# Performance work log

Measured on AMD Instinct MI355X. Metric: run time of the kernel, lower is better.

The kernel has to match this reference:

```python
import jax, jax.numpy as jnp
import numpy as np

N, C, S = 2, 512, 256
SCALE = 2.0

def setup_inputs() -> dict:
    key = jax.random.key(0)
    kq, kk, kv = jax.random.split(key, 3)
    q = jax.random.normal(kq, (N, C, S), dtype=jnp.float32)
    k = jax.random.normal(kk, (N, C, S), dtype=jnp.float32)
    v = jax.random.normal(kv, (N, C, S), dtype=jnp.float32)
    return {"q": q, "k": k, "v": v}

def reference(q, k, v):
    # q: (N,C,S) -> (N,C,1,S); k: (N,C,S) -> (N,1,C,S)
    # weights[n,c,d] = -sum_s |k[n,d,s] - q[n,c,s]| / scale
    diff = jnp.abs(k[:, None, :, :] - q[:, :, None, :])  # (N,C,C,S)
    weights = -(diff / SCALE).sum(axis=-1)               # (N,C,C)
    weights = jax.nn.softmax(weights, axis=-1)
    rep = jnp.einsum('ncd,nds->ncs', weights, v)         # (N,C,S)
    return rep
```

## Files before the change

kernel.cpp:

```cpp
#include <hip/hip_runtime.h>
#include <hip/hip_bf16.h>


constexpr int N_ = 2;
constexpr int C_ = 512;
constexpr int S_ = 256;
constexpr int TC = 4;
constexpr int NW = 4;

template <int CTRL, int ROW_MASK>
__device__ __forceinline__ float dpp_add(float x) {
    int yi = __builtin_amdgcn_update_dpp(0, __float_as_int(x), CTRL, ROW_MASK, 0xf, true);
    return x + __int_as_float(yi);
}
template <int CTRL, int ROW_MASK>
__device__ __forceinline__ float dpp_max(float x) {
    int yi = __builtin_amdgcn_update_dpp(__float_as_int(x), __float_as_int(x), CTRL, ROW_MASK, 0xf, false);
    return fmaxf(x, __int_as_float(yi));
}
__device__ __forceinline__ float dpp_reduce_halves(float x) {
    x = dpp_add<0x111, 0xf>(x);
    x = dpp_add<0x112, 0xf>(x);
    x = dpp_add<0x114, 0xf>(x);
    x = dpp_add<0x118, 0xf>(x);
    x = dpp_add<0x142, 0xa>(x);
    return x;
}
__device__ __forceinline__ float wave_sum_bcast(float x) {
    x = dpp_reduce_halves(x);
    x = dpp_add<0x143, 0xc>(x);
    return __int_as_float(__builtin_amdgcn_readlane(__float_as_int(x), 63));
}
__device__ __forceinline__ float wave_max_bcast(float x) {
    x = dpp_max<0x111, 0xf>(x);
    x = dpp_max<0x112, 0xf>(x);
    x = dpp_max<0x114, 0xf>(x);
    x = dpp_max<0x118, 0xf>(x);
    x = dpp_max<0x142, 0xa>(x);
    x = dpp_max<0x143, 0xc>(x);
    return __int_as_float(__builtin_amdgcn_readlane(__float_as_int(x), 63));
}

template <int DSPLIT>
__global__ __launch_bounds__(256, 4)
void laplace_attn_main(const float* __restrict__ q,
                       const float* __restrict__ k,
                       const float* __restrict__ v,
                       float* __restrict__ ws) {
    constexpr int DH  = C_ / DSPLIT;
    constexpr int DPW = DH / NW;
    constexpr int E   = DH / 64;
    constexpr size_t PO_SZ = (size_t)N_ * C_ * DSPLIT * S_;
    constexpr size_t ST_SZ = (size_t)N_ * C_ * DSPLIT;

    const int b      = blockIdx.x;
    constexpr int per_n = (C_ / TC) * DSPLIT;
    const int n    = b / per_n;
    const int r    = b - n * per_n;
    const int half = r % DSPLIT;
    const int c0   = (r / DSPLIT) * TC;
    const int tid  = threadIdx.x;
    const int w    = tid >> 6;
    const int lane = tid & 63;

    const float* kbase = k + (size_t)n * C_ * S_;
    const float* vbase = v + (size_t)n * C_ * S_;

    float* po = ws;
    float* pm = ws + PO_SZ;
    float* pl = pm + ST_SZ;

    __shared__ float4 wt[DH];
    __shared__ float4 accs[NW][TC][64];

    const int h = lane >> 5;
    const int j = lane & 31;
    float4 qa[TC], qb[TC];
    #pragma unroll
    for (int c = 0; c < TC; ++c) {
        const float4* qr = (const float4*)(q + ((size_t)n * C_ + c0 + c) * S_);
        qa[c] = qr[2 * j];
        qb[c] = qr[2 * j + 1];
    }

    const int dw0 = half * DH + w * DPW;
    const float* kw = kbase + (size_t)dw0 * S_;

    #pragma unroll 2
    for (int g2 = 0; g2 < DPW; g2 += 2) {
        const float4* rp = (const float4*)(kw + (size_t)(g2 + h) * S_ + j * 8);
        const float4 ka = rp[0];
        const float4 kb = rp[1];
        float s0[TC], s1[TC];
        #pragma unroll
        for (int c = 0; c < TC; ++c) {
            float p = fabsf(ka.x - qa[c].x) + fabsf(ka.y - qa[c].y)
                    + fabsf(ka.z - qa[c].z) + fabsf(ka.w - qa[c].w)
                    + fabsf(kb.x - qb[c].x) + fabsf(kb.y - qb[c].y)
                    + fabsf(kb.z - qb[c].z) + fabsf(kb.w - qb[c].w);
            p = dpp_reduce_halves(p);
            s0[c] = __int_as_float(__builtin_amdgcn_readlane(__float_as_int(p), 31));
            s1[c] = __int_as_float(__builtin_amdgcn_readlane(__float_as_int(p), 63));
        }
        if (lane == 0) {
            wt[w * DPW + g2]     = make_float4(-0.5f * s0[0], -0.5f * s0[1],
                                               -0.5f * s0[2], -0.5f * s0[3]);
            wt[w * DPW + g2 + 1] = make_float4(-0.5f * s1[0], -0.5f * s1[1],
                                               -0.5f * s1[2], -0.5f * s1[3]);
        }
    }
    __syncthreads();

    {
        const float* wtf = (const float*)wt;
        float x[E];
        #pragma unroll
        for (int e = 0; e < E; ++e) x[e] = wtf[(lane + 64 * e) * 4 + w];
        float m = x[0];
        #pragma unroll
        for (int e = 1; e < E; ++e) m = fmaxf(m, x[e]);
        m = wave_max_bcast(m);
        float es[E], l = 0.f;
        #pragma unroll
        for (int e = 0; e < E; ++e) { es[e] = __expf(x[e] - m); l += es[e]; }
        l = wave_sum_bcast(l);
        float* wtm = (float*)wt;
        #pragma unroll
        for (int e = 0; e < E; ++e) wtm[(lane + 64 * e) * 4 + w] = es[e];
        if (lane == 0) {
            const size_t sidx = ((size_t)n * C_ + c0 + w) * DSPLIT + half;
            pm[sidx] = m;
            pl[sidx] = l;
        }
    }
    __syncthreads();

    float4 acc[TC];
    #pragma unroll
    for (int c = 0; c < TC; ++c) acc[c] = make_float4(0.f, 0.f, 0.f, 0.f);

    const float4* v4 = (const float4*)(vbase + (size_t)dw0 * S_);
    #pragma unroll 4
    for (int dd = 0; dd < DPW; ++dd) {
        const float4 vv = v4[dd * 64 + lane];
        const float4 ww = wt[w * DPW + dd];
        acc[0].x += ww.x * vv.x; acc[0].y += ww.x * vv.y;
        acc[0].z += ww.x * vv.z; acc[0].w += ww.x * vv.w;
        acc[1].x += ww.y * vv.x; acc[1].y += ww.y * vv.y;
        acc[1].z += ww.y * vv.z; acc[1].w += ww.y * vv.w;
        acc[2].x += ww.z * vv.x; acc[2].y += ww.z * vv.y;
        acc[2].z += ww.z * vv.z; acc[2].w += ww.z * vv.w;
        acc[3].x += ww.w * vv.x; acc[3].y += ww.w * vv.y;
        acc[3].z += ww.w * vv.z; acc[3].w += ww.w * vv.w;
    }
    #pragma unroll
    for (int c = 0; c < TC; ++c) accs[w][c][lane] = acc[c];
    __syncthreads();

    {
        const int c = w;
        float4 a  = accs[0][c][lane];
        float4 bq = accs[1][c][lane];
        float4 cc = accs[2][c][lane];
        float4 dq = accs[3][c][lane];
        float4 o;
        o.x = (a.x + bq.x) + (cc.x + dq.x);
        o.y = (a.y + bq.y) + (cc.y + dq.y);
        o.z = (a.z + bq.z) + (cc.z + dq.z);
        o.w = (a.w + bq.w) + (cc.w + dq.w);
        const size_t oidx = (((size_t)n * C_ + c0 + c) * DSPLIT + half) * S_;
        ((float4*)(po + oidx))[lane] = o;
    }
}

template <int DSPLIT>
__global__ __launch_bounds__(64)
void laplace_attn_combine(const float* __restrict__ ws,
                          float* __restrict__ out) {
    constexpr size_t PO_SZ = (size_t)N_ * C_ * DSPLIT * S_;
    constexpr size_t ST_SZ = (size_t)N_ * C_ * DSPLIT;
    const int b    = blockIdx.x;
    const int lane = threadIdx.x;

    const float* po = ws;
    const float* pm = ws + PO_SZ;
    const float* pl = pm + ST_SZ;

    float m[DSPLIT], l[DSPLIT];
    #pragma unroll
    for (int hh = 0; hh < DSPLIT; ++hh) {
        m[hh] = pm[(size_t)b * DSPLIT + hh];
        l[hh] = pl[(size_t)b * DSPLIT + hh];
    }
    float M = m[0];
    #pragma unroll
    for (int hh = 1; hh < DSPLIT; ++hh) M = fmaxf(M, m[hh]);
    float den = 0.f, a[DSPLIT];
    #pragma unroll
    for (int hh = 0; hh < DSPLIT; ++hh) { a[hh] = __expf(m[hh] - M); den += a[hh] * l[hh]; }
    const float inv = 1.f / den;

    float4 rsum = make_float4(0.f, 0.f, 0.f, 0.f);
    #pragma unroll
    for (int hh = 0; hh < DSPLIT; ++hh) {
        const float4 o = ((const float4*)(po + ((size_t)b * DSPLIT + hh) * S_))[lane];
        rsum.x += a[hh] * o.x;
        rsum.y += a[hh] * o.y;
        rsum.z += a[hh] * o.z;
        rsum.w += a[hh] * o.w;
    }
    float4 rr;
    rr.x = rsum.x * inv; rr.y = rsum.y * inv;
    rr.z = rsum.z * inv; rr.w = rsum.w * inv;
    ((float4*)(out + (size_t)b * S_))[lane] = rr;
}

extern "C" void kernel_launch(void* const* d_in, const int* in_sizes, int n_in,
                              void* d_out, int out_size, void* d_ws, size_t ws_size,
                              hipStream_t stream) {
    const float* q = (const float*)d_in[0];
    const float* k = (const float*)d_in[1];
    const float* v = (const float*)d_in[2];
    float* out = (float*)d_out;
    float* ws  = (float*)d_ws;

    constexpr size_t NEED4 =
        ((size_t)N_ * C_ * 4 * S_ + 2 * (size_t)N_ * C_ * 4) * sizeof(float);

    if (ws_size >= NEED4) {
        laplace_attn_main<4><<<dim3(N_ * (C_ / TC) * 4), dim3(256), 0, stream>>>(q, k, v, ws);
        laplace_attn_combine<4><<<dim3(N_ * C_), dim3(64), 0, stream>>>(ws, out);
    } else {
        laplace_attn_main<2><<<dim3(N_ * (C_ / TC) * 2), dim3(256), 0, stream>>>(q, k, v, ws);
        laplace_attn_combine<2><<<dim3(N_ * C_), dim3(64), 0, stream>>>(ws, out);
    }
}
```

Measured before the change: 77.76 us.

## Fuse split-D attention into single online-softmax kernel with LDS-staged K/V chunks

Replaces the two-kernel split-D scheme (partial outputs plus a combine pass through workspace) with one fused kernel that streams K and V in 64-row chunks through shared memory and keeps an online softmax per row. This removes the workspace round trip and the second launch. The grid shrinks from 1024 or 512 blocks to 256 blocks, and each chunk needs several barriers, so parallelism and latency hiding may suffer. Each lane computes one full 256-length distance serially out of LDS instead of a cross-lane reduction.

```diff
diff --git a/kernel.cpp b/kernel.cpp
--- a/kernel.cpp
+++ b/kernel.cpp
@@ -1,12 +1,15 @@
 #include <hip/hip_runtime.h>
-#include <hip/hip_bf16.h>
 
 
-constexpr int N_ = 2;
-constexpr int C_ = 512;
-constexpr int S_ = 256;
-constexpr int TC = 4;
-constexpr int NW = 4;
+constexpr int N_  = 2;
+constexpr int C_  = 512;
+constexpr int S_  = 256;
+constexpr int S4  = S_ / 4;
+constexpr int TC  = 4;
+constexpr int DC  = 64;
+constexpr int NCH = C_ / DC;
+constexpr int KST = S_ + 4;
+constexpr int F4C = DC * S4 / 256;
 
 template <int CTRL, int ROW_MASK>
 __device__ __forceinline__ float dpp_add(float x) {
@@ -18,16 +21,12 @@
     int yi = __builtin_amdgcn_update_dpp(__float_as_int(x), __float_as_int(x), CTRL, ROW_MASK, 0xf, false);
     return fmaxf(x, __int_as_float(yi));
 }
-__device__ __forceinline__ float dpp_reduce_halves(float x) {
+__device__ __forceinline__ float wave_sum_bcast(float x) {
     x = dpp_add<0x111, 0xf>(x);
     x = dpp_add<0x112, 0xf>(x);
     x = dpp_add<0x114, 0xf>(x);
     x = dpp_add<0x118, 0xf>(x);
     x = dpp_add<0x142, 0xa>(x);
-    return x;
-}
-__device__ __forceinline__ float wave_sum_bcast(float x) {
-    x = dpp_reduce_halves(x);
     x = dpp_add<0x143, 0xc>(x);
     return __int_as_float(__builtin_amdgcn_readlane(__float_as_int(x), 63));
 }
@@ -41,178 +40,125 @@
     return __int_as_float(__builtin_amdgcn_readlane(__float_as_int(x), 63));
 }
 
-template <int DSPLIT>
-__global__ __launch_bounds__(256, 4)
-void laplace_attn_main(const float* __restrict__ q,
-                       const float* __restrict__ k,
-                       const float* __restrict__ v,
-                       float* __restrict__ ws) {
-    constexpr int DH  = C_ / DSPLIT;
-    constexpr int DPW = DH / NW;
-    constexpr int E   = DH / 64;
-    constexpr size_t PO_SZ = (size_t)N_ * C_ * DSPLIT * S_;
-    constexpr size_t ST_SZ = (size_t)N_ * C_ * DSPLIT;
+__global__ __launch_bounds__(256, 1)
+void laplace_attn_fused(const float* __restrict__ qg,
+                        const float* __restrict__ kg,
+                        const float* __restrict__ vg,
+                        float* __restrict__ out) {
+    __shared__ __align__(16) float qs[TC][S_];
+    __shared__ __align__(16) float ksm[DC][KST];
+    __shared__ __align__(16) float vsm[DC][S_];
 
-    const int b      = blockIdx.x;
-    constexpr int per_n = (C_ / TC) * DSPLIT;
-    const int n    = b / per_n;
-    const int r    = b - n * per_n;
-    const int half = r % DSPLIT;
-    const int c0   = (r / DSPLIT) * TC;
+    const int b    = blockIdx.x;
+    const int n    = b & 1;
+    const int c0   = (b >> 1) * TC;
     const int tid  = threadIdx.x;
     const int w    = tid >> 6;
     const int lane = tid & 63;
 
-    const float* kbase = k + (size_t)n * C_ * S_;
-    const float* vbase = v + (size_t)n * C_ * S_;
+    const float* kn = kg + (size_t)n * C_ * S_;
+    const float* vn = vg + (size_t)n * C_ * S_;
 
-    float* po = ws;
-    float* pm = ws + PO_SZ;
-    float* pl = pm + ST_SZ;
-
-    __shared__ float4 wt[DH];
-    __shared__ float4 accs[NW][TC][64];
-
-    const int h = lane >> 5;
-    const int j = lane & 31;
-    float4 qa[TC], qb[TC];
+    float4 kreg[F4C];
     #pragma unroll
-    for (int c = 0; c < TC; ++c) {
-        const float4* qr = (const float4*)(q + ((size_t)n * C_ + c0 + c) * S_);
-        qa[c] = qr[2 * j];
-        qb[c] = qr[2 * j + 1];
+    for (int it = 0; it < F4C; ++it) {
+        const int f   = tid + 256 * it;
+        const int row = f >> 6;
+        const int c4  = f & 63;
+        kreg[it] = *(const float4*)(kn + (size_t)row * S_ + (c4 << 2));
     }
-
-    const int dw0 = half * DH + w * DPW;
-    const float* kw = kbase + (size_t)dw0 * S_;
-
-    #pragma unroll 2
-    for (int g2 = 0; g2 < DPW; g2 += 2) {
-        const float4* rp = (const float4*)(kw + (size_t)(g2 + h) * S_ + j * 8);
-        const float4 ka = rp[0];
-        const float4 kb = rp[1];
-        float s0[TC], s1[TC];
-        #pragma unroll
-        for (int c = 0; c < TC; ++c) {
-            float p = fabsf(ka.x - qa[c].x) + fabsf(ka.y - qa[c].y)
-                    + fabsf(ka.z - qa[c].z) + fabsf(ka.w - qa[c].w)
-                    + fabsf(kb.x - qb[c].x) + fabsf(kb.y - qb[c].y)
-                    + fabsf(kb.z - qb[c].z) + fabsf(kb.w - qb[c].w);
-            p = dpp_reduce_halves(p);
-            s0[c] = __int_as_float(__builtin_amdgcn_readlane(__float_as_int(p), 31));
-            s1[c] = __int_as_float(__builtin_amdgcn_readlane(__float_as_int(p), 63));
-        }
-        if (lane == 0) {
-            wt[w * DPW + g2]     = make_float4(-0.5f * s0[0], -0.5f * s0[1],
-                                               -0.5f * s0[2], -0.5f * s0[3]);
-            wt[w * DPW + g2 + 1] = make_float4(-0.5f * s1[0], -0.5f * s1[1],
-                                               -0.5f * s1[2], -0.5f * s1[3]);
-        }
+    {
+        const float4 qv = *(const float4*)(qg + ((size_t)n * C_ + c0 + w) * S_ + (lane << 2));
+        *(float4*)&qs[w][lane << 2] = qv;
+    }
+    #pragma unroll
+    for (int it = 0; it < F4C; ++it) {
+        const int f   = tid + 256 * it;
+        const int row = f >> 6;
+        const int c4  = f & 63;
+        *(float4*)&ksm[row][c4 << 2] = kreg[it];
     }
     __syncthreads();
 
-    {
-        const float* wtf = (const float*)wt;
-        float x[E];
+    float  m_run = -3.402823466e+38f;
+    float  l_run = 0.f;
+    float4 o = make_float4(0.f, 0.f, 0.f, 0.f);
+
+    for (int ch = 0; ch < NCH; ++ch) {
+        const int d0 = ch * DC;
+
+        float4 vreg[F4C];
         #pragma unroll
-        for (int e = 0; e < E; ++e) x[e] = wtf[(lane + 64 * e) * 4 + w];
-        float m = x[0];
+        for (int it = 0; it < F4C; ++it) {
+            const int f   = tid + 256 * it;
+            const int row = f >> 6;
+            const int c4  = f & 63;
+            vreg[it] = *(const float4*)(vn + (size_t)(d0 + row) * S_ + (c4 << 2));
+        }
+
+        float dist = 0.f;
         #pragma unroll
-        for (int e = 1; e < E; ++e) m = fmaxf(m, x[e]);
-        m = wave_max_bcast(m);
-        float es[E], l = 0.f;
+        for (int s4 = 0; s4 < S4; ++s4) {
+            const float4 kf = *(const float4*)&ksm[lane][s4 << 2];
+            const float4 qf = *(const float4*)&qs[w][s4 << 2];
+            dist += (fabsf(kf.x - qf.x) + fabsf(kf.y - qf.y))
+                  + (fabsf(kf.z - qf.z) + fabsf(kf.w - qf.w));
+        }
+
+        const float x     = -0.5f * dist;
+        const float Mc    = wave_max_bcast(x);
+        const float m_new = fmaxf(m_run, Mc);
+        const float aa    = __expf(m_run - m_new);
+        const float p     = __expf(x - m_new);
+        const float ls    = wave_sum_bcast(p);
+        l_run = l_run * aa + ls;
+        m_run = m_new;
+        o.x *= aa; o.y *= aa; o.z *= aa; o.w *= aa;
+
+        __syncthreads();
+
         #pragma unroll
-        for (int e = 0; e < E; ++e) { es[e] = __expf(x[e] - m); l += es[e]; }
-        l = wave_sum_bcast(l);
-        float* wtm = (float*)wt;
+        for (int it = 0; it < F4C; ++it) {
+            const int f   = tid + 256 * it;
+            const int row = f >> 6;
+            const int c4  = f & 63;
+            *(float4*)&vsm[row][c4 << 2] = vreg[it];
+        }
+        if (ch + 1 < NCH) {
+            #pragma unroll
+            for (int it = 0; it < F4C; ++it) {
+                const int f   = tid + 256 * it;
+                const int row = f >> 6;
+                const int c4  = f & 63;
+                kreg[it] = *(const float4*)(kn + (size_t)(d0 + DC + row) * S_ + (c4 << 2));
+            }
+        }
+        __syncthreads();
+
         #pragma unroll
-        for (int e = 0; e < E; ++e) wtm[(lane + 64 * e) * 4 + w] = es[e];
-        if (lane == 0) {
-            const size_t sidx = ((size_t)n * C_ + c0 + w) * DSPLIT + half;
-            pm[sidx] = m;
-            pl[sidx] = l;
+        for (int dd = 0; dd < DC; ++dd) {
+            const float pd = __int_as_float(__builtin_amdgcn_readlane(__float_as_int(p), dd));
+            const float4 vv = *(const float4*)&vsm[dd][lane << 2];
+            o.x += pd * vv.x; o.y += pd * vv.y;
+            o.z += pd * vv.z; o.w += pd * vv.w;
         }
+
+        if (ch + 1 < NCH) {
+            #pragma unroll
+            for (int it = 0; it < F4C; ++it) {
+                const int f   = tid + 256 * it;
+                const int row = f >> 6;
+                const int c4  = f & 63;
+                *(float4*)&ksm[row][c4 << 2] = kreg[it];
+            }
+        }
+        __syncthreads();
     }
-    __syncthreads();
 
-    float4 acc[TC];
-    #pragma unroll
-    for (int c = 0; c < TC; ++c) acc[c] = make_float4(0.f, 0.f, 0.f, 0.f);
-
-    const float4* v4 = (const float4*)(vbase + (size_t)dw0 * S_);
-    #pragma unroll 4
-    for (int dd = 0; dd < DPW; ++dd) {
-        const float4 vv = v4[dd * 64 + lane];
-        const float4 ww = wt[w * DPW + dd];
-        acc[0].x += ww.x * vv.x; acc[0].y += ww.x * vv.y;
-        acc[0].z += ww.x * vv.z; acc[0].w += ww.x * vv.w;
-        acc[1].x += ww.y * vv.x; acc[1].y += ww.y * vv.y;
-        acc[1].z += ww.y * vv.z; acc[1].w += ww.y * vv.w;
-        acc[2].x += ww.z * vv.x; acc[2].y += ww.z * vv.y;
-        acc[2].z += ww.z * vv.z; acc[2].w += ww.z * vv.w;
-        acc[3].x += ww.w * vv.x; acc[3].y += ww.w * vv.y;
-        acc[3].z += ww.w * vv.z; acc[3].w += ww.w * vv.w;
-    }
-    #pragma unroll
-    for (int c = 0; c < TC; ++c) accs[w][c][lane] = acc[c];
-    __syncthreads();
-
-    {
-        const int c = w;
-        float4 a  = accs[0][c][lane];
-        float4 bq = accs[1][c][lane];
-        float4 cc = accs[2][c][lane];
-        float4 dq = accs[3][c][lane];
-        float4 o;
-        o.x = (a.x + bq.x) + (cc.x + dq.x);
-        o.y = (a.y + bq.y) + (cc.y + dq.y);
-        o.z = (a.z + bq.z) + (cc.z + dq.z);
-        o.w = (a.w + bq.w) + (cc.w + dq.w);
-        const size_t oidx = (((size_t)n * C_ + c0 + c) * DSPLIT + half) * S_;
-        ((float4*)(po + oidx))[lane] = o;
-    }
-}
-
-template <int DSPLIT>
-__global__ __launch_bounds__(64)
-void laplace_attn_combine(const float* __restrict__ ws,
-                          float* __restrict__ out) {
-    constexpr size_t PO_SZ = (size_t)N_ * C_ * DSPLIT * S_;
-    constexpr size_t ST_SZ = (size_t)N_ * C_ * DSPLIT;
-    const int b    = blockIdx.x;
-    const int lane = threadIdx.x;
-
-    const float* po = ws;
-    const float* pm = ws + PO_SZ;
-    const float* pl = pm + ST_SZ;
-
-    float m[DSPLIT], l[DSPLIT];
-    #pragma unroll
-    for (int hh = 0; hh < DSPLIT; ++hh) {
-        m[hh] = pm[(size_t)b * DSPLIT + hh];
-        l[hh] = pl[(size_t)b * DSPLIT + hh];
-    }
-    float M = m[0];
-    #pragma unroll
-    for (int hh = 1; hh < DSPLIT; ++hh) M = fmaxf(M, m[hh]);
-    float den = 0.f, a[DSPLIT];
-    #pragma unroll
-    for (int hh = 0; hh < DSPLIT; ++hh) { a[hh] = __expf(m[hh] - M); den += a[hh] * l[hh]; }
-    const float inv = 1.f / den;
-
-    float4 rsum = make_float4(0.f, 0.f, 0.f, 0.f);
-    #pragma unroll
-    for (int hh = 0; hh < DSPLIT; ++hh) {
-        const float4 o = ((const float4*)(po + ((size_t)b * DSPLIT + hh) * S_))[lane];
-        rsum.x += a[hh] * o.x;
-        rsum.y += a[hh] * o.y;
-        rsum.z += a[hh] * o.z;
-        rsum.w += a[hh] * o.w;
-    }
-    float4 rr;
-    rr.x = rsum.x * inv; rr.y = rsum.y * inv;
-    rr.z = rsum.z * inv; rr.w = rsum.w * inv;
-    ((float4*)(out + (size_t)b * S_))[lane] = rr;
+    const float inv = 1.f / l_run;
+    float4 r;
+    r.x = o.x * inv; r.y = o.y * inv; r.z = o.z * inv; r.w = o.w * inv;
+    *(float4*)(out + ((size_t)n * C_ + c0 + w) * S_ + (lane << 2)) = r;
 }
 
 extern "C" void kernel_launch(void* const* d_in, const int* in_sizes, int n_in,
@@ -222,16 +168,7 @@
     const float* k = (const float*)d_in[1];
     const float* v = (const float*)d_in[2];
     float* out = (float*)d_out;
-    float* ws  = (float*)d_ws;
+    (void)d_ws; (void)ws_size;
 
-    constexpr size_t NEED4 =
-        ((size_t)N_ * C_ * 4 * S_ + 2 * (size_t)N_ * C_ * 4) * sizeof(float);
-
-    if (ws_size >= NEED4) {
-        laplace_attn_main<4><<<dim3(N_ * (C_ / TC) * 4), dim3(256), 0, stream>>>(q, k, v, ws);
-        laplace_attn_combine<4><<<dim3(N_ * C_), dim3(64), 0, stream>>>(ws, out);
-    } else {
-        laplace_attn_main<2><<<dim3(N_ * (C_ / TC) * 2), dim3(256), 0, stream>>>(q, k, v, ws);
-        laplace_attn_combine<2><<<dim3(N_ * C_), dim3(64), 0, stream>>>(ws, out);
-    }
+    laplace_attn_fused<<<dim3(N_ * (C_ / TC)), dim3(256), 0, stream>>>(q, k, v, out);
 }
```

New measurement: 165.7 us. 2.13x slower.
